# Kernel tuning notes

Measured on AMD Instinct MI355X. Metric: run time of the kernel, lower is better.

The kernel has to match this reference:

```python
import jax, jax.numpy as jnp
import numpy as np

EPS = 1e-8

def cos_sim(a, b, axis=-1):
    # torch.nn.functional.cosine_similarity: dot / max(|a|*|b|, eps)
    num = jnp.sum(a * b, axis=axis)
    den = jnp.maximum(jnp.linalg.norm(a, axis=axis) * jnp.linalg.norm(b, axis=axis), EPS)
    return num / den

def address_similarity(address, addresses):
    # address: [b, d], addresses: [b, n, d] -> [b, n]
    return cos_sim(address[:, None, :], addresses, axis=2)

def kv_insert(state_k, state_v, k, x, eps=EPS):
    # state_k/state_v: [b, n, d]; k: [b, d]; x: [b, d] (or [1, d], broadcast)
    alpha = cos_sim(k[:, None, :], state_k, axis=2)          # [b, n]
    alpha = jnp.where(alpha > eps, alpha, 0.0)
    return (1.0 - alpha)[..., None] * state_v + alpha[..., None] * x[:, None, :]

def replace(new_value, prev_value, tensr):
    # new_value/prev_value: [b, d]; tensr: [b, n, d]
    sim_to = cos_sim(prev_value[:, None, :], tensr, axis=2)  # [b, n]
    return tensr * (1.0 - sim_to)[..., None] + sim_to[..., None] * new_value[:, None, :]

def select_address(address, addresses, list_of_values):
    cs = address_similarity(address, addresses)              # [b, n]
    return [jnp.sum(values * cs[..., None], axis=1) for values in list_of_values]

def setup_inputs() -> dict:
    key = jax.random.key(0)
    ks = jax.random.split(key, 5)
    B, N, D = 32, 2048, 128
    return {
        "at_addr": jax.random.normal(ks[0], (B, D), dtype=jnp.float32),
        "addresses": jax.random.normal(ks[1], (B, N, D), dtype=jnp.float32),
        "tags": jax.random.normal(ks[2], (B, N, D), dtype=jnp.float32),
        "col1": jax.random.normal(ks[3], (B, N, D), dtype=jnp.float32),
        "col2": jax.random.normal(ks[4], (B, N, D), dtype=jnp.float32),
        "zero_vec": jnp.zeros((D,), dtype=jnp.float32),
        "gc_steps": 2,
    }

def reference(at_addr, addresses, tags, col1, col2, zero_vec, gc_steps):
    B = at_addr.shape[0]
    zv = jnp.broadcast_to(zero_vec[None, :], (B, zero_vec.shape[0]))
    # dereference the App node
    fn_addr, arg_addr = select_address(at_addr, addresses, [col1, col2])
    fn_tag, param_addr, body_addr = select_address(fn_addr, addresses, [tags, col1, col2])
    a_tag, a_l, a_r = select_address(arg_addr, addresses, [tags, col1, col2])
    # substitute arg into param's slot (globally scoped vars)
    tags = kv_insert(addresses, tags, param_addr, a_tag)
    col1 = kv_insert(addresses, col1, param_addr, a_l)
    col2 = kv_insert(addresses, col2, param_addr, a_r)
    col1 = replace(arg_addr, param_addr, col1)
    col2 = replace(arg_addr, param_addr, col2)
    # write the fn body over the App node
    b_tag, b_l, b_r = select_address(body_addr, addresses, [tags, col1, col2])
    tags = kv_insert(addresses, tags, at_addr, b_tag)
    col1 = kv_insert(addresses, col1, at_addr, b_l)
    col2 = kv_insert(addresses, col2, at_addr, b_r)
    # garbage collection
    for _ in range(gc_steps):
        for gaddr in (fn_addr, param_addr, body_addr):
            tags = kv_insert(addresses, tags, gaddr, zv)
            col1 = kv_insert(addresses, col1, gaddr, zv)
            col2 = kv_insert(addresses, col2, gaddr, zv)
    return (tags, col1, col2)
```

## Files before the change

### kernel.cpp

```cpp
#include <hip/hip_runtime.h>

#define EPSF 1e-8f
#define DD 128

__device__ __forceinline__ float4 ld4(const float* p){ return *reinterpret_cast<const float4*>(p); }
__device__ __forceinline__ void st4(float* p, const float4& v){ *reinterpret_cast<float4*>(p) = v; }
__device__ __forceinline__ float dot4(const float4& a, const float4& b){
  return a.x*b.x + a.y*b.y + a.z*b.z + a.w*b.w;
}
__device__ __forceinline__ void fma4(float4& acc, const float4& a, float s){
  acc.x += a.x*s; acc.y += a.y*s; acc.z += a.z*s; acc.w += a.w*s;
}
__device__ __forceinline__ float4 mix4(float a, const float4& v, const float4& x){
  float4 r;
  r.x = (1.f-a)*v.x + a*x.x;
  r.y = (1.f-a)*v.y + a*x.y;
  r.z = (1.f-a)*v.z + a*x.z;
  r.w = (1.f-a)*v.w + a*x.w;
  return r;
}
__device__ __forceinline__ float red32(float v){
  v += __shfl_xor(v, 1);
  v += __shfl_xor(v, 2);
  v += __shfl_xor(v, 4);
  v += __shfl_xor(v, 8);
  v += __shfl_xor(v, 16);
  return v;
}
__device__ __forceinline__ void block_red(float* red, int group, int l, int t,
                                          const float4& acc, float* dst){
  red[group*DD + l*4+0] = acc.x;
  red[group*DD + l*4+1] = acc.y;
  red[group*DD + l*4+2] = acc.z;
  red[group*DD + l*4+3] = acc.w;
  __syncthreads();
  if (t < DD){
    float s = 0.f;
    #pragma unroll
    for (int g = 0; g < 8; ++g) s += red[g*DD + t];
    dst[t] = s;
  }
  __syncthreads();
}

__global__ __launch_bounds__(256) void kA(const float* __restrict__ at,
                                          const float* __restrict__ addr,
                                          const float* __restrict__ col1,
                                          const float* __restrict__ col2,
                                          float* __restrict__ cs0,
                                          float* __restrict__ part,
                                          int B, int N, int chunks){
  __shared__ float red[8*DD];
  int blk = blockIdx.x;
  int b = blk / chunks, c = blk % chunks;
  int rows = N / chunks, n0 = c * rows;
  int t = threadIdx.x, lane = t & 63, wave = t >> 6, l = lane & 31;
  int group = wave*2 + (lane >> 5);

  float4 at4 = ld4(at + (size_t)b*DD + l*4);
  float nat = sqrtf(red32(dot4(at4, at4)));

  float4 accF = make_float4(0,0,0,0), accA = make_float4(0,0,0,0);
  for (int r = group; r < rows; r += 8){
    size_t n = (size_t)n0 + r;
    size_t off = ((size_t)b*N + n)*DD + l*4;
    float4 a4 = ld4(addr + off);
    float dp = red32(dot4(at4, a4));
    float n2 = red32(dot4(a4, a4));
    float cs = dp / fmaxf(nat * sqrtf(n2), EPSF);
    if (l == 0) cs0[(size_t)b*N + n] = cs;
    float4 c1 = ld4(col1 + off), c2 = ld4(col2 + off);
    fma4(accF, c1, cs);
    fma4(accA, c2, cs);
  }
  block_red(red, group, l, t, accF, part + (((size_t)(0*B + b))*chunks + c)*DD);
  block_red(red, group, l, t, accA, part + (((size_t)(1*B + b))*chunks + c)*DD);
}

__global__ void kFin(const float* __restrict__ part, float* __restrict__ dst,
                     int nvec, int B, int chunks){
  int i = blockIdx.x*blockDim.x + threadIdx.x;
  int total = nvec * B * DD;
  if (i >= total) return;
  int d = i & (DD-1);
  int vb = i >> 7;
  const float* p = part + ((size_t)vb*chunks)*DD + d;
  float s = 0.f;
  for (int c = 0; c < chunks; ++c) s += p[(size_t)c*DD];
  dst[i] = s;
}

__global__ __launch_bounds__(256) void kB(const float* __restrict__ addr,
                                          const float* __restrict__ tags,
                                          const float* __restrict__ col1,
                                          const float* __restrict__ col2,
                                          const float* __restrict__ vecs,
                                          float* __restrict__ csfn,
                                          float* __restrict__ part,
                                          int B, int N, int chunks){
  __shared__ float red[8*DD];
  int blk = blockIdx.x;
  int b = blk / chunks, c = blk % chunks;
  int rows = N / chunks, n0 = c * rows;
  int t = threadIdx.x, lane = t & 63, wave = t >> 6, l = lane & 31;
  int group = wave*2 + (lane >> 5);

  float4 fn4 = ld4(vecs + ((size_t)0*B + b)*DD + l*4);
  float4 ag4 = ld4(vecs + ((size_t)1*B + b)*DD + l*4);
  float nfn = sqrtf(red32(dot4(fn4, fn4)));
  float nag = sqrtf(red32(dot4(ag4, ag4)));

  float4 accP = make_float4(0,0,0,0), accB = accP, accT = accP, accL = accP, accR = accP;
  for (int r = group; r < rows; r += 8){
    size_t n = (size_t)n0 + r;
    size_t off = ((size_t)b*N + n)*DD + l*4;
    float4 a4 = ld4(addr + off);
    float dfn = red32(dot4(fn4, a4));
    float dag = red32(dot4(ag4, a4));
    float n2  = red32(dot4(a4, a4));
    float na = sqrtf(n2);
    float cf = dfn / fmaxf(nfn*na, EPSF);
    float ca = dag / fmaxf(nag*na, EPSF);
    if (l == 0) csfn[(size_t)b*N + n] = cf;
    float4 t4 = ld4(tags + off), c1 = ld4(col1 + off), c2 = ld4(col2 + off);
    fma4(accP, c1, cf);
    fma4(accB, c2, cf);
    fma4(accT, t4, ca);
    fma4(accL, c1, ca);
    fma4(accR, c2, ca);
  }
  block_red(red, group, l, t, accP, part + (((size_t)(0*B + b))*chunks + c)*DD);
  block_red(red, group, l, t, accB, part + (((size_t)(1*B + b))*chunks + c)*DD);
  block_red(red, group, l, t, accT, part + (((size_t)(2*B + b))*chunks + c)*DD);
  block_red(red, group, l, t, accL, part + (((size_t)(3*B + b))*chunks + c)*DD);
  block_red(red, group, l, t, accR, part + (((size_t)(4*B + b))*chunks + c)*DD);
}

__global__ __launch_bounds__(256) void kC(const float* __restrict__ addr,
                                          const float* __restrict__ tags,
                                          const float* __restrict__ col1,
                                          const float* __restrict__ col2,
                                          const float* __restrict__ vecs,
                                          float* __restrict__ alphap,
                                          float* __restrict__ csbody,
                                          float* __restrict__ o_t,
                                          float* __restrict__ o_1,
                                          float* __restrict__ o_2,
                                          float* __restrict__ part,
                                          int B, int N, int chunks){
  __shared__ float red[8*DD];
  int blk = blockIdx.x;
  int b = blk / chunks, c = blk % chunks;
  int rows = N / chunks, n0 = c * rows;
  int t = threadIdx.x, lane = t & 63, wave = t >> 6, l = lane & 31;
  int group = wave*2 + (lane >> 5);

  size_t BD = (size_t)B*DD;
  float4 ag4 = ld4(vecs + 1*BD + (size_t)b*DD + l*4);
  float4 pm4 = ld4(vecs + 2*BD + (size_t)b*DD + l*4);
  float4 bd4 = ld4(vecs + 3*BD + (size_t)b*DD + l*4);
  float4 xt4 = ld4(vecs + 4*BD + (size_t)b*DD + l*4);
  float4 xl4 = ld4(vecs + 5*BD + (size_t)b*DD + l*4);
  float4 xr4 = ld4(vecs + 6*BD + (size_t)b*DD + l*4);
  float npm = sqrtf(red32(dot4(pm4, pm4)));
  float nbd = sqrtf(red32(dot4(bd4, bd4)));

  float4 accT = make_float4(0,0,0,0), accL = accT, accR = accT;
  for (int r = group; r < rows; r += 8){
    size_t n = (size_t)n0 + r;
    size_t off = ((size_t)b*N + n)*DD + l*4;
    float4 a4 = ld4(addr + off);
    float dp  = red32(dot4(pm4, a4));
    float db  = red32(dot4(bd4, a4));
    float n2a = red32(dot4(a4, a4));
    float na = sqrtf(n2a);
    float csp = dp / fmaxf(npm*na, EPSF);
    float ap  = csp > EPSF ? csp : 0.f;
    float csb = db / fmaxf(nbd*na, EPSF);
    if (l == 0){ alphap[(size_t)b*N + n] = ap; csbody[(size_t)b*N + n] = csb; }

    float4 t4 = ld4(tags + off), c1 = ld4(col1 + off), c2 = ld4(col2 + off);
    float4 tn  = mix4(ap, t4, xt4);
    float4 c1n = mix4(ap, c1, xl4);
    float4 c2n = mix4(ap, c2, xr4);
    float d1  = red32(dot4(pm4, c1n));
    float n21 = red32(dot4(c1n, c1n));
    float s1 = d1 / fmaxf(npm * sqrtf(n21), EPSF);
    float4 c1f = mix4(s1, c1n, ag4);
    float d2  = red32(dot4(pm4, c2n));
    float n22 = red32(dot4(c2n, c2n));
    float s2 = d2 / fmaxf(npm * sqrtf(n22), EPSF);
    float4 c2f = mix4(s2, c2n, ag4);

    st4(o_t + off, tn);
    st4(o_1 + off, c1f);
    st4(o_2 + off, c2f);
    fma4(accT, tn,  csb);
    fma4(accL, c1f, csb);
    fma4(accR, c2f, csb);
  }
  block_red(red, group, l, t, accT, part + (((size_t)(0*B + b))*chunks + c)*DD);
  block_red(red, group, l, t, accL, part + (((size_t)(1*B + b))*chunks + c)*DD);
  block_red(red, group, l, t, accR, part + (((size_t)(2*B + b))*chunks + c)*DD);
}

__global__ __launch_bounds__(256) void kD(float* __restrict__ o_t,
                                          float* __restrict__ o_1,
                                          float* __restrict__ o_2,
                                          const float* __restrict__ cs0,
                                          const float* __restrict__ csfn,
                                          const float* __restrict__ alphap,
                                          const float* __restrict__ csbody,
                                          const float* __restrict__ vecs,
                                          const float* __restrict__ zv,
                                          const int* __restrict__ gcp,
                                          int B, int N){
  size_t i = (size_t)blockIdx.x*blockDim.x + threadIdx.x;
  size_t total = (size_t)B*N*(DD/4);
  if (i >= total) return;
  int l = (int)(i & 31);
  size_t bn = i >> 5;
  int b = (int)(bn / (size_t)N);

  float c0 = cs0[bn], cf = csfn[bn], ap = alphap[bn], cb = csbody[bn];
  float aat = c0 > EPSF ? c0 : 0.f;
  float af  = cf > EPSF ? cf : 0.f;
  float ab  = cb > EPSF ? cb : 0.f;
  float q = (1.f-af)*(1.f-ap)*(1.f-ab);
  int gc = gcp[0];
  float P = 1.f;
  for (int k = 0; k < gc; ++k) P *= q;

  size_t BD = (size_t)B*DD;
  const float* vb = vecs + 7*BD + (size_t)b*DD + l*4;
  float4 bt = ld4(vb), bl = ld4(vb + BD), br = ld4(vb + 2*BD);
  float4 z4 = ld4(zv + l*4);

  size_t off = bn*DD + (size_t)l*4;
  float4 v, u;
  v = ld4(o_t + off); u = mix4(aat, v, bt);
  u.x = P*u.x + (1.f-P)*z4.x; u.y = P*u.y + (1.f-P)*z4.y;
  u.z = P*u.z + (1.f-P)*z4.z; u.w = P*u.w + (1.f-P)*z4.w;
  st4(o_t + off, u);
  v = ld4(o_1 + off); u = mix4(aat, v, bl);
  u.x = P*u.x + (1.f-P)*z4.x; u.y = P*u.y + (1.f-P)*z4.y;
  u.z = P*u.z + (1.f-P)*z4.z; u.w = P*u.w + (1.f-P)*z4.w;
  st4(o_1 + off, u);
  v = ld4(o_2 + off); u = mix4(aat, v, br);
  u.x = P*u.x + (1.f-P)*z4.x; u.y = P*u.y + (1.f-P)*z4.y;
  u.z = P*u.z + (1.f-P)*z4.z; u.w = P*u.w + (1.f-P)*z4.w;
  st4(o_2 + off, u);
}

extern "C" void kernel_launch(void* const* d_in, const int* in_sizes, int n_in,
                              void* d_out, int out_size, void* d_ws, size_t ws_size,
                              hipStream_t stream){
  const float* at   = (const float*)d_in[0];
  const float* addr = (const float*)d_in[1];
  const float* tags = (const float*)d_in[2];
  const float* col1 = (const float*)d_in[3];
  const float* col2 = (const float*)d_in[4];
  const float* zv   = (const float*)d_in[5];
  const int*   gc   = (const int*)d_in[6];

  int Dd = in_sizes[5];
  int B  = in_sizes[0] / Dd;
  int N  = in_sizes[1] / in_sizes[0];
  (void)Dd;

  float* w = (float*)d_ws;
  size_t S  = (size_t)B * N;
  size_t BD = (size_t)B * DD;
  float* cs0    = w;
  float* csfn   = w + S;
  float* alphap = w + 2*S;
  float* csbody = w + 3*S;
  float* vecs   = w + 4*S;
  float* part   = vecs + 10*BD;

  float* o_t = (float*)d_out;
  float* o_1 = o_t + (size_t)B*N*DD;
  float* o_2 = o_1 + (size_t)B*N*DD;

  const int CH = 32;
  dim3 blk(256);
  dim3 grid(B*CH);

  kA<<<grid, blk, 0, stream>>>(at, addr, col1, col2, cs0, part, B, N, CH);
  {
    int tot = 2*B*DD;
    kFin<<<(tot+255)/256, 256, 0, stream>>>(part, vecs + 0*BD, 2, B, CH);
  }
  kB<<<grid, blk, 0, stream>>>(addr, tags, col1, col2, vecs, csfn, part, B, N, CH);
  {
    int tot = 5*B*DD;
    kFin<<<(tot+255)/256, 256, 0, stream>>>(part, vecs + 2*BD, 5, B, CH);
  }
  kC<<<grid, blk, 0, stream>>>(addr, tags, col1, col2, vecs, alphap, csbody,
                               o_t, o_1, o_2, part, B, N, CH);
  {
    int tot = 3*B*DD;
    kFin<<<(tot+255)/256, 256, 0, stream>>>(part, vecs + 7*BD, 3, B, CH);
  }
  {
    size_t tot = (size_t)B*N*(DD/4);
    kD<<<(unsigned)((tot+255)/256), 256, 0, stream>>>(o_t, o_1, o_2, cs0, csfn, alphap,
                                                      csbody, vecs, zv, gc, B, N);
  }
}
```

Measured before the change: 139.2 us.

## Stop storing intermediate state in kC; recompute it from inputs in final kernel

kC no longer writes the full updated tags/col1/col2 tensors to the output. It stores only the per-row scalars (alpha, body similarity, replace similarities), and the final kernel rebuilds the updated rows from the original inputs. This trades one full-tensor write and reread for an input reread, cutting global memory traffic. It also caches per-row address norms from kA so later kernels skip one reduction, and it raises the chunk count from 32 to 64 when the workspace allows.

```diff
diff --git a/kernel.cpp b/kernel.cpp
--- a/kernel.cpp
+++ b/kernel.cpp
@@ -48,6 +48,7 @@
                                           const float* __restrict__ col1,
                                           const float* __restrict__ col2,
                                           float* __restrict__ cs0,
+                                          float* __restrict__ naf,
                                           float* __restrict__ part,
                                           int B, int N, int chunks){
   __shared__ float red[8*DD];
@@ -65,11 +66,12 @@
     size_t n = (size_t)n0 + r;
     size_t off = ((size_t)b*N + n)*DD + l*4;
     float4 a4 = ld4(addr + off);
+    float4 c1 = ld4(col1 + off), c2 = ld4(col2 + off);
     float dp = red32(dot4(at4, a4));
     float n2 = red32(dot4(a4, a4));
-    float cs = dp / fmaxf(nat * sqrtf(n2), EPSF);
-    if (l == 0) cs0[(size_t)b*N + n] = cs;
-    float4 c1 = ld4(col1 + off), c2 = ld4(col2 + off);
+    float na = sqrtf(n2);
+    float cs = dp / fmaxf(nat * na, EPSF);
+    if (l == 0){ cs0[(size_t)b*N + n] = cs; naf[(size_t)b*N + n] = na; }
     fma4(accF, c1, cs);
     fma4(accA, c2, cs);
   }
@@ -95,6 +97,7 @@
                                           const float* __restrict__ col1,
                                           const float* __restrict__ col2,
                                           const float* __restrict__ vecs,
+                                          const float* __restrict__ naf,
                                           float* __restrict__ csfn,
                                           float* __restrict__ part,
                                           int B, int N, int chunks){
@@ -115,14 +118,13 @@
     size_t n = (size_t)n0 + r;
     size_t off = ((size_t)b*N + n)*DD + l*4;
     float4 a4 = ld4(addr + off);
+    float4 t4 = ld4(tags + off), c1 = ld4(col1 + off), c2 = ld4(col2 + off);
+    float na = naf[(size_t)b*N + n];
     float dfn = red32(dot4(fn4, a4));
     float dag = red32(dot4(ag4, a4));
-    float n2  = red32(dot4(a4, a4));
-    float na = sqrtf(n2);
     float cf = dfn / fmaxf(nfn*na, EPSF);
     float ca = dag / fmaxf(nag*na, EPSF);
     if (l == 0) csfn[(size_t)b*N + n] = cf;
-    float4 t4 = ld4(tags + off), c1 = ld4(col1 + off), c2 = ld4(col2 + off);
     fma4(accP, c1, cf);
     fma4(accB, c2, cf);
     fma4(accT, t4, ca);
@@ -141,11 +143,11 @@
                                           const float* __restrict__ col1,
                                           const float* __restrict__ col2,
                                           const float* __restrict__ vecs,
+                                          const float* __restrict__ naf,
                                           float* __restrict__ alphap,
                                           float* __restrict__ csbody,
-                                          float* __restrict__ o_t,
-                                          float* __restrict__ o_1,
-                                          float* __restrict__ o_2,
+                                          float* __restrict__ s1f,
+                                          float* __restrict__ s2f,
                                           float* __restrict__ part,
                                           int B, int N, int chunks){
   __shared__ float red[8*DD];
@@ -170,16 +172,14 @@
     size_t n = (size_t)n0 + r;
     size_t off = ((size_t)b*N + n)*DD + l*4;
     float4 a4 = ld4(addr + off);
+    float4 t4 = ld4(tags + off), c1 = ld4(col1 + off), c2 = ld4(col2 + off);
+    float na = naf[(size_t)b*N + n];
     float dp  = red32(dot4(pm4, a4));
     float db  = red32(dot4(bd4, a4));
-    float n2a = red32(dot4(a4, a4));
-    float na = sqrtf(n2a);
     float csp = dp / fmaxf(npm*na, EPSF);
     float ap  = csp > EPSF ? csp : 0.f;
     float csb = db / fmaxf(nbd*na, EPSF);
-    if (l == 0){ alphap[(size_t)b*N + n] = ap; csbody[(size_t)b*N + n] = csb; }
-
-    float4 t4 = ld4(tags + off), c1 = ld4(col1 + off), c2 = ld4(col2 + off);
+
     float4 tn  = mix4(ap, t4, xt4);
     float4 c1n = mix4(ap, c1, xl4);
     float4 c2n = mix4(ap, c2, xr4);
@@ -192,9 +192,12 @@
     float s2 = d2 / fmaxf(npm * sqrtf(n22), EPSF);
     float4 c2f = mix4(s2, c2n, ag4);
 
-    st4(o_t + off, tn);
-    st4(o_1 + off, c1f);
-    st4(o_2 + off, c2f);
+    if (l == 0){
+      alphap[(size_t)b*N + n] = ap;
+      csbody[(size_t)b*N + n] = csb;
+      s1f[(size_t)b*N + n] = s1;
+      s2f[(size_t)b*N + n] = s2;
+    }
     fma4(accT, tn,  csb);
     fma4(accL, c1f, csb);
     fma4(accR, c2f, csb);
@@ -204,13 +207,18 @@
   block_red(red, group, l, t, accR, part + (((size_t)(2*B + b))*chunks + c)*DD);
 }
 
-__global__ __launch_bounds__(256) void kD(float* __restrict__ o_t,
+__global__ __launch_bounds__(256) void kE(const float* __restrict__ tags,
+                                          const float* __restrict__ col1,
+                                          const float* __restrict__ col2,
+                                          float* __restrict__ o_t,
                                           float* __restrict__ o_1,
                                           float* __restrict__ o_2,
                                           const float* __restrict__ cs0,
                                           const float* __restrict__ csfn,
                                           const float* __restrict__ alphap,
                                           const float* __restrict__ csbody,
+                                          const float* __restrict__ s1f,
+                                          const float* __restrict__ s2f,
                                           const float* __restrict__ vecs,
                                           const float* __restrict__ zv,
                                           const int* __restrict__ gcp,
@@ -222,7 +230,8 @@
   size_t bn = i >> 5;
   int b = (int)(bn / (size_t)N);
 
-  float c0 = cs0[bn], cf = csfn[bn], ap = alphap[bn], cb = csbody[bn];
+  float ap = alphap[bn], s1 = s1f[bn], s2 = s2f[bn];
+  float c0 = cs0[bn], cf = csfn[bn], cb = csbody[bn];
   float aat = c0 > EPSF ? c0 : 0.f;
   float af  = cf > EPSF ? cf : 0.f;
   float ab  = cb > EPSF ? cb : 0.f;
@@ -232,21 +241,29 @@
   for (int k = 0; k < gc; ++k) P *= q;
 
   size_t BD = (size_t)B*DD;
-  const float* vb = vecs + 7*BD + (size_t)b*DD + l*4;
-  float4 bt = ld4(vb), bl = ld4(vb + BD), br = ld4(vb + 2*BD);
+  const float* vb = vecs + (size_t)b*DD + (size_t)l*4;
+  float4 ag = ld4(vb + 1*BD);
+  float4 xt = ld4(vb + 4*BD), xl = ld4(vb + 5*BD), xr = ld4(vb + 6*BD);
+  float4 bt = ld4(vb + 7*BD), bl = ld4(vb + 8*BD), br = ld4(vb + 9*BD);
   float4 z4 = ld4(zv + l*4);
 
   size_t off = bn*DD + (size_t)l*4;
-  float4 v, u;
-  v = ld4(o_t + off); u = mix4(aat, v, bt);
+  float4 t4 = ld4(tags + off), c1 = ld4(col1 + off), c2 = ld4(col2 + off);
+
+  float4 tn  = mix4(ap, t4, xt);
+  float4 c1f = mix4(s1, mix4(ap, c1, xl), ag);
+  float4 c2f = mix4(s2, mix4(ap, c2, xr), ag);
+
+  float4 u;
+  u = mix4(aat, tn, bt);
   u.x = P*u.x + (1.f-P)*z4.x; u.y = P*u.y + (1.f-P)*z4.y;
   u.z = P*u.z + (1.f-P)*z4.z; u.w = P*u.w + (1.f-P)*z4.w;
   st4(o_t + off, u);
-  v = ld4(o_1 + off); u = mix4(aat, v, bl);
+  u = mix4(aat, c1f, bl);
   u.x = P*u.x + (1.f-P)*z4.x; u.y = P*u.y + (1.f-P)*z4.y;
   u.z = P*u.z + (1.f-P)*z4.z; u.w = P*u.w + (1.f-P)*z4.w;
   st4(o_1 + off, u);
-  v = ld4(o_2 + off); u = mix4(aat, v, br);
+  u = mix4(aat, c2f, br);
   u.x = P*u.x + (1.f-P)*z4.x; u.y = P*u.y + (1.f-P)*z4.y;
   u.z = P*u.z + (1.f-P)*z4.z; u.w = P*u.w + (1.f-P)*z4.w;
   st4(o_2 + off, u);
@@ -268,43 +285,54 @@
   int N  = in_sizes[1] / in_sizes[0];
   (void)Dd;
 
-  float* w = (float*)d_ws;
   size_t S  = (size_t)B * N;
   size_t BD = (size_t)B * DD;
+
+  int CH = 64;
+  while (CH > 1){
+    size_t need = (7*S + 10*BD + (size_t)5*B*CH*DD) * sizeof(float);
+    if (need <= ws_size && (N % CH) == 0) break;
+    CH >>= 1;
+  }
+
+  float* w = (float*)d_ws;
   float* cs0    = w;
   float* csfn   = w + S;
   float* alphap = w + 2*S;
   float* csbody = w + 3*S;
-  float* vecs   = w + 4*S;
+  float* s1f    = w + 4*S;
+  float* s2f    = w + 5*S;
+  float* naf    = w + 6*S;
+  float* vecs   = w + 7*S;
   float* part   = vecs + 10*BD;
 
   float* o_t = (float*)d_out;
   float* o_1 = o_t + (size_t)B*N*DD;
   float* o_2 = o_1 + (size_t)B*N*DD;
 
-  const int CH = 32;
   dim3 blk(256);
   dim3 grid(B*CH);
 
-  kA<<<grid, blk, 0, stream>>>(at, addr, col1, col2, cs0, part, B, N, CH);
+  kA<<<grid, blk, 0, stream>>>(at, addr, col1, col2, cs0, naf, part, B, N, CH);
   {
     int tot = 2*B*DD;
     kFin<<<(tot+255)/256, 256, 0, stream>>>(part, vecs + 0*BD, 2, B, CH);
   }
-  kB<<<grid, blk, 0, stream>>>(addr, tags, col1, col2, vecs, csfn, part, B, N, CH);
+  kB<<<grid, blk, 0, stream>>>(addr, tags, col1, col2, vecs, naf, csfn, part, B, N, CH);
   {
     int tot = 5*B*DD;
     kFin<<<(tot+255)/256, 256, 0, stream>>>(part, vecs + 2*BD, 5, B, CH);
   }
-  kC<<<grid, blk, 0, stream>>>(addr, tags, col1, col2, vecs, alphap, csbody,
-                               o_t, o_1, o_2, part, B, N, CH);
+  kC<<<grid, blk, 0, stream>>>(addr, tags, col1, col2, vecs, naf, alphap, csbody,
+                               s1f, s2f, part, B, N, CH);
   {
     int tot = 3*B*DD;
     kFin<<<(tot+255)/256, 256, 0, stream>>>(part, vecs + 7*BD, 3, B, CH);
   }
   {
     size_t tot = (size_t)B*N*(DD/4);
-    kD<<<(unsigned)((tot+255)/256), 256, 0, stream>>>(o_t, o_1, o_2, cs0, csfn, alphap,
-                                                      csbody, vecs, zv, gc, B, N);
-  }
-}
+    kE<<<(unsigned)((tot+255)/256), 256, 0, stream>>>(tags, col1, col2, o_t, o_1, o_2,
+                                                      cs0, csfn, alphap, csbody,
+                                                      s1f, s2f, vecs, zv, gc, B, N);
+  }
+}
```

Result: slower. 152.8 us (+9.8%).
